# Optimization experiments

Measured on AMD Instinct MI355X. Metric: run time of the kernel, lower is better.

The kernel has to match this reference:

```python
import jax, jax.numpy as jnp
import numpy as np

NUM_HEADS = 16


def setup_inputs() -> dict:
    key = jax.random.key(0)
    k1, k2, k3 = jax.random.split(key, 3)
    b, d, s = 2, 1024, 2048
    x = jax.random.normal(k1, (b, d, s), dtype=jnp.float32)
    # torch nn.Linear(d, 3d) without bias == x @ W1 with W1 of shape (d, 3d)
    W1 = jax.random.normal(k2, (d, 3 * d), dtype=jnp.float32) * (d ** -0.5)
    W2 = jax.random.normal(k3, (d, d), dtype=jnp.float32) * (d ** -0.5)
    return {"x": x, "W1": W1, "W2": W2}


def reference(x, W1, W2):
    # x: (b, hidden_dim, s) -> (b, s, hidden_dim)
    b, d, s = x.shape
    h = NUM_HEADS
    hd = d // h
    xt = jnp.swapaxes(x, 1, 2)                       # (b, s, d)
    qkv = xt @ W1                                    # (b, s, 3d)
    qkv = qkv.reshape(b, s, 3, h, hd)
    qkv = jnp.transpose(qkv, (2, 0, 3, 1, 4))        # (3, b, h, s, hd)
    q, k, v = qkv[0], qkv[1], qkv[2]
    scale = hd ** -0.5
    scores = jnp.einsum("bhqd,bhkd->bhqk", q, k) * scale  # (b, h, s, s)
    # causal mask: same as torch code (adds float32 min where not lower-tri)
    neg = jnp.finfo(jnp.float32).min
    causal = jnp.tril(jnp.ones((s, s), dtype=bool))
    scores = jnp.where(causal[None, None, :, :], scores, scores + neg)
    attn = jax.nn.softmax(scores, axis=-1)           # dropout = identity (eval)
    out = jnp.einsum("bhqk,bhkd->bhqd", attn, v)     # (b, h, s, hd)
    out = jnp.transpose(out, (0, 2, 1, 3)).reshape(b, s, d)
    out = out @ W2                                   # (b, s, d)
    return jnp.swapaxes(out, 1, 2)                   # (b, d, s)
```

## Files before the change

kernel.cpp:

```cpp
#include <hip/hip_runtime.h>
#include <math.h>

#define B_  2
#define D_  1024
#define S_  2048
#define H_  16
#define HD_ 64
#define D3_ 3072
#define M_  4096

typedef __attribute__((ext_vector_type(8))) short short8;
typedef __attribute__((ext_vector_type(4))) float float4v;

__device__ __forceinline__ short f2bf(float f) {
    unsigned u = __builtin_bit_cast(unsigned, f);
    unsigned r = (u + 0x7FFFu + ((u >> 16) & 1u)) >> 16;
    return (short)r;
}

__device__ __forceinline__ unsigned cvt_pk_bf16(float lo, float hi) {
    unsigned r;
    asm("v_cvt_pk_bf16_f32 %0, %1, %2" : "=v"(r) : "v"(lo), "v"(hi));
    return r;
}

__device__ __forceinline__ float fast_exp2(float x) {
    float r;
    asm("v_exp_f32 %0, %1" : "=v"(r) : "v"(x));
    return r;
}

#define GLD16(gsrc, ldst)                                                      \
    __builtin_amdgcn_global_load_lds(                                          \
        (const __attribute__((address_space(1))) void*)(gsrc),                 \
        (__attribute__((address_space(3))) void*)(ldst), 16, 0, 0)

__global__ __launch_bounds__(256) void transpose_cvt(const float* __restrict__ in,
                                                     short* __restrict__ out,
                                                     int R, int C) {
    __shared__ float t[32][33];
    const int c0 = blockIdx.x * 32, r0 = blockIdx.y * 32;
    const float* inb = in + (size_t)blockIdx.z * R * C;
    short* outb = out + (size_t)blockIdx.z * R * C;
    const int tx = threadIdx.x, ty = threadIdx.y;
    #pragma unroll
    for (int i = ty; i < 32; i += 8)
        t[i][tx] = inb[(size_t)(r0 + i) * C + c0 + tx];
    __syncthreads();
    #pragma unroll
    for (int i = ty; i < 32; i += 8)
        outb[(size_t)(c0 + i) * R + r0 + tx] = f2bf(t[tx][i]);
}

__device__ __forceinline__ void gemm_core(const short* __restrict__ A,
                                          const short* __restrict__ Bt,
                                          int m0, int n0,
                                          short* As, short* Bs,
                                          float4v acc[4][4]) {
    const int tid = threadIdx.x;
    const int lane = tid & 63, w = tid >> 6;
    const int wr = (w >> 1) * 64, wc = (w & 1) * 64;
    const int srow = lane >> 2;
    const int scol = (lane & 3) * 8;
    for (int k0 = 0; k0 < 1024; k0 += 32) {
        #pragma unroll
        for (int j = 0; j < 2; ++j) {
            const int ch = 2 * w + j;
            GLD16(A  + (size_t)(m0 + ch * 16 + srow) * 1024 + k0 + scol,
                  As + ch * 512 + lane * 8);
            GLD16(Bt + (size_t)(n0 + ch * 16 + srow) * 1024 + k0 + scol,
                  Bs + ch * 512 + lane * 8);
        }
        __syncthreads();
        short8 a[4], b[4];
        #pragma unroll
        for (int m = 0; m < 4; ++m)
            a[m] = *(const short8*)&As[(wr + m * 16 + (lane & 15)) * 32 + (lane >> 4) * 8];
        #pragma unroll
        for (int n = 0; n < 4; ++n)
            b[n] = *(const short8*)&Bs[(wc + n * 16 + (lane & 15)) * 32 + (lane >> 4) * 8];
        #pragma unroll
        for (int m = 0; m < 4; ++m)
            #pragma unroll
            for (int n = 0; n < 4; ++n)
                acc[m][n] = __builtin_amdgcn_mfma_f32_16x16x32_bf16(a[m], b[n], acc[m][n], 0, 0, 0);
        __syncthreads();
    }
}

__global__ __launch_bounds__(256) void gemm_qkv_mfma(const short* __restrict__ xt,
                                                     const short* __restrict__ W1t,
                                                     short* __restrict__ q,
                                                     short* __restrict__ kk,
                                                     short* __restrict__ vt) {
    __shared__ short As[128 * 32], Bs[128 * 32];
    float4v acc[4][4];
    #pragma unroll
    for (int m = 0; m < 4; ++m)
        #pragma unroll
        for (int n = 0; n < 4; ++n) acc[m][n] = (float4v){0.f, 0.f, 0.f, 0.f};
    const int m0 = blockIdx.y * 128, n0 = blockIdx.x * 128;
    gemm_core(xt, W1t, m0, n0, As, Bs, acc);
    const int lane = threadIdx.x & 63, w = threadIdx.x >> 6;
    const int wr = (w >> 1) * 64, wc = (w & 1) * 64;
    const float qscale = 0.125f * 1.44269504f;
    #pragma unroll
    for (int n = 0; n < 4; ++n) {
        const int gcol = n0 + wc + n * 16 + (lane & 15);
        const int which = gcol >> 10, hh = (gcol >> 6) & 15, hd = gcol & 63;
        #pragma unroll
        for (int m = 0; m < 4; ++m) {
            #pragma unroll
            for (int ri = 0; ri < 4; ++ri) {
                const int grow = m0 + wr + m * 16 + (lane >> 4) * 4 + ri;
                const int bb = grow >> 11, ss = grow & (S_ - 1);
                float av = acc[m][n][ri];
                if (which == 0) av *= qscale;
                const short v = f2bf(av);
                if (which == 0)      q [((size_t)(bb * H_ + hh) * S_ + ss) * HD_ + hd] = v;
                else if (which == 1) kk[((size_t)(bb * H_ + hh) * S_ + ss) * HD_ + hd] = v;
                else                 vt[((size_t)(bb * H_ + hh) * HD_ + hd) * S_ + ss] = v;
            }
        }
    }
}

__global__ __launch_bounds__(256) void attn_mfma(const short* __restrict__ q,
                                                 const short* __restrict__ k,
                                                 const short* __restrict__ vt,
                                                 short* __restrict__ ao) {
    __shared__ short Ks[2][64 * 64];
    __shared__ short Vts[2][64 * 64];
    __shared__ short Ps[64 * 64];
    __shared__ float sums[64];
    const int tid = threadIdx.x;
    const int lane = tid & 63, w = tid >> 6;
    const int bh = blockIdx.y;
    const size_t base = (size_t)bh * S_ * HD_;
    const short* qp = q + base;
    const short* kp = k + base;
    const short* vp = vt + base;
    const int bb = bh >> 4, hh = bh & 15;
    const int wrow = w * 16;

    for (int half = 0; half < 2; ++half) {
        const int qt = (half == 0) ? (int)blockIdx.x : 31 - (int)blockIdx.x;
        const int q0 = qt * 64;
        short8 qf[2];
        #pragma unroll
        for (int ks = 0; ks < 2; ++ks)
            qf[ks] = *(const short8*)&qp[(size_t)(q0 + wrow + (lane & 15)) * HD_
                                         + ks * 32 + (lane >> 4) * 8];
        float4v accO[4];
        float lsum = 0.f;
        #pragma unroll
        for (int n = 0; n < 4; ++n) accO[n] = (float4v){0.f, 0.f, 0.f, 0.f};

        const int nkb = qt + 1;
        __syncthreads();
        #pragma unroll
        for (int j = 0; j < 2; ++j) {
            const int g = (w * 2 + j) * 64 + lane;
            const int r = g >> 3, cs = g & 7;
            const int co = (cs ^ (r & 7)) << 3;
            GLD16(kp + (size_t)r * HD_ + co, &Ks[0][g * 8]);
            GLD16(vp + (size_t)r * S_ + co,  &Vts[0][g * 8]);
        }
        int cur = 0;
        for (int kb = 0; kb < nkb; ++kb) {
            const int kv0 = kb * 64;
            __syncthreads();
            if (kb + 1 < nkb) {
                const int kv1 = kv0 + 64;
                #pragma unroll
                for (int j = 0; j < 2; ++j) {
                    const int g = (w * 2 + j) * 64 + lane;
                    const int r = g >> 3, cs = g & 7;
                    const int co = (cs ^ (r & 7)) << 3;
                    GLD16(kp + (size_t)(kv1 + r) * HD_ + co, &Ks[cur ^ 1][g * 8]);
                    GLD16(vp + (size_t)r * S_ + kv1 + co,    &Vts[cur ^ 1][g * 8]);
                }
            }
            float4v accS[4];
            #pragma unroll
            for (int n = 0; n < 4; ++n) accS[n] = (float4v){0.f, 0.f, 0.f, 0.f};
            #pragma unroll
            for (int ks = 0; ks < 2; ++ks) {
                #pragma unroll
                for (int n = 0; n < 4; ++n) {
                    const int rowk = n * 16 + (lane & 15);
                    const int ch = ks * 4 + (lane >> 4);
                    const short8 kf = *(const short8*)&Ks[cur][rowk * 64 + ((ch ^ (rowk & 7)) << 3)];
                    accS[n] = __builtin_amdgcn_mfma_f32_16x16x32_bf16(kf, qf[ks], accS[n], 0, 0, 0);
                }
            }
            const bool diag = (kb == qt);
            const int qg = q0 + wrow + (lane & 15);
            const int prow = wrow + (lane & 15);
            #pragma unroll
            for (int n = 0; n < 4; ++n) {
                const int kvb = kv0 + n * 16 + ((lane >> 4) << 2);
                float p[4];
                if (diag) {
                    const int dlim = qg - kvb;
                    #pragma unroll
                    for (int ri = 0; ri < 4; ++ri)
                        p[ri] = (ri <= dlim) ? fast_exp2(accS[n][ri]) : 0.f;
                } else {
                    #pragma unroll
                    for (int ri = 0; ri < 4; ++ri)
                        p[ri] = fast_exp2(accS[n][ri]);
                }
                lsum += (p[0] + p[1]) + (p[2] + p[3]);
                const unsigned lo = cvt_pk_bf16(p[0], p[1]);
                const unsigned hi = cvt_pk_bf16(p[2], p[3]);
                const int col = n * 16 + ((lane >> 4) << 2);
                const int ch = col >> 3;
                const int addr = prow * 64 + ((ch ^ (prow & 7)) << 3) + (col & 7);
                *(uint2*)&Ps[addr] = (uint2){lo, hi};
            }
            #pragma unroll
            for (int ks = 0; ks < 2; ++ks) {
                const int prow2 = wrow + (lane & 15);
                const int chp = ks * 4 + (lane >> 4);
                const short8 pf = *(const short8*)&Ps[prow2 * 64 + ((chp ^ (prow2 & 7)) << 3)];
                #pragma unroll
                for (int n = 0; n < 4; ++n) {
                    const int vrow = n * 16 + (lane & 15);
                    const int ch = ks * 4 + (lane >> 4);
                    const short8 vf = *(const short8*)&Vts[cur][vrow * 64 + ((ch ^ (vrow & 7)) << 3)];
                    accO[n] = __builtin_amdgcn_mfma_f32_16x16x32_bf16(pf, vf, accO[n], 0, 0, 0);
                }
            }
            cur ^= 1;
        }
        {
            float t = lsum;
            t += __shfl_xor(t, 16);
            t += __shfl_xor(t, 32);
            if (lane < 16) sums[wrow + lane] = t;
        }
        #pragma unroll
        for (int ri = 0; ri < 4; ++ri) {
            const int lrow = wrow + ((lane >> 4) << 2) + ri;
            const float inv = 1.f / sums[lrow];
            const int grow = q0 + lrow;
            #pragma unroll
            for (int n = 0; n < 4; ++n) {
                const int col = hh * 64 + n * 16 + (lane & 15);
                ao[((size_t)(bb * S_ + grow)) * D_ + col] = f2bf(accO[n][ri] * inv);
            }
        }
    }
}

__global__ __launch_bounds__(256) void gemm_out_mfma(const short* __restrict__ W2t,
                                                     const short* __restrict__ ao,
                                                     float* __restrict__ out) {
    __shared__ short As[128 * 32], Bs[128 * 32];
    float4v acc[4][4];
    #pragma unroll
    for (int m = 0; m < 4; ++m)
        #pragma unroll
        for (int n = 0; n < 4; ++n) acc[m][n] = (float4v){0.f, 0.f, 0.f, 0.f};
    const int m0 = blockIdx.y * 128, n0 = blockIdx.x * 128;
    gemm_core(W2t, ao, m0, n0, As, Bs, acc);
    const int lane = threadIdx.x & 63, w = threadIdx.x >> 6;
    const int wr = (w >> 1) * 64, wc = (w & 1) * 64;
    #pragma unroll
    for (int m = 0; m < 4; ++m) {
        #pragma unroll
        for (int ri = 0; ri < 4; ++ri) {
            const int grow = m0 + wr + m * 16 + (lane >> 4) * 4 + ri;
            #pragma unroll
            for (int n = 0; n < 4; ++n) {
                const int gcol = n0 + wc + n * 16 + (lane & 15);
                const int bb = gcol >> 11, ss = gcol & (S_ - 1);
                out[(size_t)bb * D_ * S_ + (size_t)grow * S_ + ss] = acc[m][n][ri];
            }
        }
    }
}

extern "C" void kernel_launch(void* const* d_in, const int* in_sizes, int n_in,
                              void* d_out, int out_size, void* d_ws, size_t ws_size,
                              hipStream_t stream) {
    const float* x  = (const float*)d_in[0];
    const float* W1 = (const float*)d_in[1];
    const float* W2 = (const float*)d_in[2];
    float* out = (float*)d_out;

    short* xt  = (short*)d_ws;
    short* W1t = xt  + (size_t)M_ * D_;
    short* W2t = W1t + (size_t)D3_ * D_;
    short* q   = W2t + (size_t)D_ * D_;
    short* kk  = q   + (size_t)B_ * H_ * S_ * HD_;
    short* vt  = kk  + (size_t)B_ * H_ * S_ * HD_;
    short* ao  = vt  + (size_t)B_ * H_ * S_ * HD_;

    transpose_cvt<<<dim3(S_ / 32, D_ / 32, B_), dim3(32, 8), 0, stream>>>(x, xt, D_, S_);
    transpose_cvt<<<dim3(D3_ / 32, D_ / 32, 1), dim3(32, 8), 0, stream>>>(W1, W1t, D_, D3_);
    transpose_cvt<<<dim3(D_ / 32, D_ / 32, 1), dim3(32, 8), 0, stream>>>(W2, W2t, D_, D_);
    gemm_qkv_mfma<<<dim3(D3_ / 128, M_ / 128), 256, 0, stream>>>(xt, W1t, q, kk, vt);
    attn_mfma<<<dim3(16, B_ * H_), 256, 0, stream>>>(q, kk, vt, ao);
    gemm_out_mfma<<<dim3(M_ / 128, D_ / 128), 256, 0, stream>>>(W2t, ao, out);
}
```

Measured before the change: 129.6 us.

## Double-buffer GEMM LDS tiles and add XCD-aware block swizzle

```diff
diff --git a/kernel.cpp b/kernel.cpp
--- a/kernel.cpp
+++ b/kernel.cpp
@@ -62,30 +62,47 @@
     const int wr = (w >> 1) * 64, wc = (w & 1) * 64;
     const int srow = lane >> 2;
     const int scol = (lane & 3) * 8;
-    for (int k0 = 0; k0 < 1024; k0 += 32) {
-        #pragma unroll
-        for (int j = 0; j < 2; ++j) {
-            const int ch = 2 * w + j;
-            GLD16(A  + (size_t)(m0 + ch * 16 + srow) * 1024 + k0 + scol,
-                  As + ch * 512 + lane * 8);
-            GLD16(Bt + (size_t)(n0 + ch * 16 + srow) * 1024 + k0 + scol,
-                  Bs + ch * 512 + lane * 8);
-        }
+    #pragma unroll
+    for (int j = 0; j < 2; ++j) {
+        const int ch = 2 * w + j;
+        GLD16(A  + (size_t)(m0 + ch * 16 + srow) * 1024 + scol, As + ch * 512 + lane * 8);
+        GLD16(Bt + (size_t)(n0 + ch * 16 + srow) * 1024 + scol, Bs + ch * 512 + lane * 8);
+    }
+    int cur = 0;
+    for (int t = 0; t < 32; ++t) {
         __syncthreads();
+        if (t + 1 < 32) {
+            const int k1 = (t + 1) * 32;
+            short* Asn = As + (cur ^ 1) * 4096;
+            short* Bsn = Bs + (cur ^ 1) * 4096;
+            #pragma unroll
+            for (int j = 0; j < 2; ++j) {
+                const int ch = 2 * w + j;
+                GLD16(A  + (size_t)(m0 + ch * 16 + srow) * 1024 + k1 + scol, Asn + ch * 512 + lane * 8);
+                GLD16(Bt + (size_t)(n0 + ch * 16 + srow) * 1024 + k1 + scol, Bsn + ch * 512 + lane * 8);
+            }
+        }
+        const short* Asc = As + cur * 4096;
+        const short* Bsc = Bs + cur * 4096;
         short8 a[4], b[4];
         #pragma unroll
         for (int m = 0; m < 4; ++m)
-            a[m] = *(const short8*)&As[(wr + m * 16 + (lane & 15)) * 32 + (lane >> 4) * 8];
+            a[m] = *(const short8*)&Asc[(wr + m * 16 + (lane & 15)) * 32 + (lane >> 4) * 8];
         #pragma unroll
         for (int n = 0; n < 4; ++n)
-            b[n] = *(const short8*)&Bs[(wc + n * 16 + (lane & 15)) * 32 + (lane >> 4) * 8];
+            b[n] = *(const short8*)&Bsc[(wc + n * 16 + (lane & 15)) * 32 + (lane >> 4) * 8];
         #pragma unroll
         for (int m = 0; m < 4; ++m)
             #pragma unroll
             for (int n = 0; n < 4; ++n)
                 acc[m][n] = __builtin_amdgcn_mfma_f32_16x16x32_bf16(a[m], b[n], acc[m][n], 0, 0, 0);
-        __syncthreads();
-    }
+        cur ^= 1;
+    }
+}
+
+__device__ __forceinline__ int xcd_swizzle(int bid, int nwg) {
+    const int cpx = nwg >> 3;
+    return (bid & 7) * cpx + (bid >> 3);
 }
 
 __global__ __launch_bounds__(256) void gemm_qkv_mfma(const short* __restrict__ xt,
@@ -93,14 +110,15 @@
                                                      short* __restrict__ q,
                                                      short* __restrict__ kk,
                                                      short* __restrict__ vt) {
-    __shared__ short As[128 * 32], Bs[128 * 32];
+    __shared__ short As[2][128 * 32], Bs[2][128 * 32];
     float4v acc[4][4];
     #pragma unroll
     for (int m = 0; m < 4; ++m)
         #pragma unroll
         for (int n = 0; n < 4; ++n) acc[m][n] = (float4v){0.f, 0.f, 0.f, 0.f};
-    const int m0 = blockIdx.y * 128, n0 = blockIdx.x * 128;
-    gemm_core(xt, W1t, m0, n0, As, Bs, acc);
+    const int bid = xcd_swizzle((int)blockIdx.x, 24 * 32);
+    const int m0 = (bid / 24) * 128, n0 = (bid % 24) * 128;
+    gemm_core(xt, W1t, m0, n0, &As[0][0], &Bs[0][0], acc);
     const int lane = threadIdx.x & 63, w = threadIdx.x >> 6;
     const int wr = (w >> 1) * 64, wc = (w & 1) * 64;
     const float qscale = 0.125f * 1.44269504f;
@@ -257,14 +275,15 @@
 __global__ __launch_bounds__(256) void gemm_out_mfma(const short* __restrict__ W2t,
                                                      const short* __restrict__ ao,
                                                      float* __restrict__ out) {
-    __shared__ short As[128 * 32], Bs[128 * 32];
+    __shared__ short As[2][128 * 32], Bs[2][128 * 32];
     float4v acc[4][4];
     #pragma unroll
     for (int m = 0; m < 4; ++m)
         #pragma unroll
         for (int n = 0; n < 4; ++n) acc[m][n] = (float4v){0.f, 0.f, 0.f, 0.f};
-    const int m0 = blockIdx.y * 128, n0 = blockIdx.x * 128;
-    gemm_core(W2t, ao, m0, n0, As, Bs, acc);
+    const int bid = xcd_swizzle((int)blockIdx.x, 8 * 32);
+    const int m0 = (bid / 32) * 128, n0 = (bid % 32) * 128;
+    gemm_core(W2t, ao, m0, n0, &As[0][0], &Bs[0][0], acc);
     const int lane = threadIdx.x & 63, w = threadIdx.x >> 6;
     const int wr = (w >> 1) * 64, wc = (w & 1) * 64;
     #pragma unroll
@@ -301,7 +320,7 @@
     transpose_cvt<<<dim3(S_ / 32, D_ / 32, B_), dim3(32, 8), 0, stream>>>(x, xt, D_, S_);
     transpose_cvt<<<dim3(D3_ / 32, D_ / 32, 1), dim3(32, 8), 0, stream>>>(W1, W1t, D_, D3_);
     transpose_cvt<<<dim3(D_ / 32, D_ / 32, 1), dim3(32, 8), 0, stream>>>(W2, W2t, D_, D_);
-    gemm_qkv_mfma<<<dim3(D3_ / 128, M_ / 128), 256, 0, stream>>>(xt, W1t, q, kk, vt);
+    gemm_qkv_mfma<<<dim3(24 * 32), 256, 0, stream>>>(xt, W1t, q, kk, vt);
     attn_mfma<<<dim3(16, B_ * H_), 256, 0, stream>>>(q, kk, vt, ao);
-    gemm_out_mfma<<<dim3(M_ / 128, D_ / 128), 256, 0, stream>>>(W2t, ao, out);
-}
+    gemm_out_mfma<<<dim3(8 * 32), 256, 0, stream>>>(W2t, ao, out);
+}
```

After: 137.2 us. 1.06x slower.

## Double GEMM K-tile to 64 with XOR-swizzled LDS and remap attention blocks per XCD

Applied to the files above, without the earlier changes.

```diff
diff --git a/kernel.cpp b/kernel.cpp
--- a/kernel.cpp
+++ b/kernel.cpp
@@ -60,30 +60,37 @@
     const int tid = threadIdx.x;
     const int lane = tid & 63, w = tid >> 6;
     const int wr = (w >> 1) * 64, wc = (w & 1) * 64;
-    const int srow = lane >> 2;
-    const int scol = (lane & 3) * 8;
-    for (int k0 = 0; k0 < 1024; k0 += 32) {
-        #pragma unroll
-        for (int j = 0; j < 2; ++j) {
-            const int ch = 2 * w + j;
-            GLD16(A  + (size_t)(m0 + ch * 16 + srow) * 1024 + k0 + scol,
-                  As + ch * 512 + lane * 8);
-            GLD16(Bt + (size_t)(n0 + ch * 16 + srow) * 1024 + k0 + scol,
-                  Bs + ch * 512 + lane * 8);
+    for (int k0 = 0; k0 < 1024; k0 += 64) {
+        #pragma unroll
+        for (int j = 0; j < 4; ++j) {
+            const int g = j * 256 + tid;
+            const int r = g >> 3, cs = g & 7;
+            const int co = (cs ^ (r & 7)) << 3;
+            GLD16(A  + (size_t)(m0 + r) * 1024 + k0 + co, As + g * 8);
+            GLD16(Bt + (size_t)(n0 + r) * 1024 + k0 + co, Bs + g * 8);
         }
         __syncthreads();
-        short8 a[4], b[4];
-        #pragma unroll
-        for (int m = 0; m < 4; ++m)
-            a[m] = *(const short8*)&As[(wr + m * 16 + (lane & 15)) * 32 + (lane >> 4) * 8];
-        #pragma unroll
-        for (int n = 0; n < 4; ++n)
-            b[n] = *(const short8*)&Bs[(wc + n * 16 + (lane & 15)) * 32 + (lane >> 4) * 8];
-        #pragma unroll
-        for (int m = 0; m < 4; ++m)
-            #pragma unroll
-            for (int n = 0; n < 4; ++n)
-                acc[m][n] = __builtin_amdgcn_mfma_f32_16x16x32_bf16(a[m], b[n], acc[m][n], 0, 0, 0);
+        #pragma unroll
+        for (int ks = 0; ks < 2; ++ks) {
+            short8 a[4], b[4];
+            #pragma unroll
+            for (int m = 0; m < 4; ++m) {
+                const int row = wr + m * 16 + (lane & 15);
+                const int ch = ks * 4 + (lane >> 4);
+                a[m] = *(const short8*)&As[row * 64 + ((ch ^ (row & 7)) << 3)];
+            }
+            #pragma unroll
+            for (int n = 0; n < 4; ++n) {
+                const int row = wc + n * 16 + (lane & 15);
+                const int ch = ks * 4 + (lane >> 4);
+                b[n] = *(const short8*)&Bs[row * 64 + ((ch ^ (row & 7)) << 3)];
+            }
+            #pragma unroll
+            for (int m = 0; m < 4; ++m)
+                #pragma unroll
+                for (int n = 0; n < 4; ++n)
+                    acc[m][n] = __builtin_amdgcn_mfma_f32_16x16x32_bf16(a[m], b[n], acc[m][n], 0, 0, 0);
+        }
         __syncthreads();
     }
 }
@@ -93,7 +100,7 @@
                                                      short* __restrict__ q,
                                                      short* __restrict__ kk,
                                                      short* __restrict__ vt) {
-    __shared__ short As[128 * 32], Bs[128 * 32];
+    __shared__ short As[128 * 64], Bs[128 * 64];
     float4v acc[4][4];
     #pragma unroll
     for (int m = 0; m < 4; ++m)
@@ -135,7 +142,10 @@
     __shared__ float sums[64];
     const int tid = threadIdx.x;
     const int lane = tid & 63, w = tid >> 6;
-    const int bh = blockIdx.y;
+    const int bid = (int)blockIdx.x;
+    const int xcd = bid & 7, slot = bid >> 3;
+    const int bh = xcd * 4 + (slot & 3);
+    const int qpair = slot >> 2;
     const size_t base = (size_t)bh * S_ * HD_;
     const short* qp = q + base;
     const short* kp = k + base;
@@ -144,7 +154,7 @@
     const int wrow = w * 16;
 
     for (int half = 0; half < 2; ++half) {
-        const int qt = (half == 0) ? (int)blockIdx.x : 31 - (int)blockIdx.x;
+        const int qt = (half == 0) ? qpair : 31 - qpair;
         const int q0 = qt * 64;
         short8 qf[2];
         #pragma unroll
@@ -257,7 +267,7 @@
 __global__ __launch_bounds__(256) void gemm_out_mfma(const short* __restrict__ W2t,
                                                      const short* __restrict__ ao,
                                                      float* __restrict__ out) {
-    __shared__ short As[128 * 32], Bs[128 * 32];
+    __shared__ short As[128 * 64], Bs[128 * 64];
     float4v acc[4][4];
     #pragma unroll
     for (int m = 0; m < 4; ++m)
@@ -302,6 +312,6 @@
     transpose_cvt<<<dim3(D3_ / 32, D_ / 32, 1), dim3(32, 8), 0, stream>>>(W1, W1t, D_, D3_);
     transpose_cvt<<<dim3(D_ / 32, D_ / 32, 1), dim3(32, 8), 0, stream>>>(W2, W2t, D_, D_);
     gemm_qkv_mfma<<<dim3(D3_ / 128, M_ / 128), 256, 0, stream>>>(xt, W1t, q, kk, vt);
-    attn_mfma<<<dim3(16, B_ * H_), 256, 0, stream>>>(q, kk, vt, ao);
+    attn_mfma<<<dim3(512), 256, 0, stream>>>(q, kk, vt, ao);
     gemm_out_mfma<<<dim3(M_ / 128, D_ / 128), 256, 0, stream>>>(W2t, ao, out);
 }
```

Result: slower. 134.0 us (+3.4%).

## Process paired short and long query tiles together to share K/V loads

Applied to the files above, without the earlier changes.

```diff
diff --git a/kernel.cpp b/kernel.cpp
--- a/kernel.cpp
+++ b/kernel.cpp
@@ -131,10 +131,11 @@
                                                  short* __restrict__ ao) {
     __shared__ short Ks[2][64 * 64];
     __shared__ short Vts[2][64 * 64];
-    __shared__ short Ps[64 * 64];
-    __shared__ float sums[64];
+    __shared__ short Ps[128 * 64];
+    __shared__ float sums[128];
     const int tid = threadIdx.x;
     const int lane = tid & 63, w = tid >> 6;
+    const int qpair = blockIdx.x;
     const int bh = blockIdx.y;
     const size_t base = (size_t)bh * S_ * HD_;
     const short* qp = q + base;
@@ -143,60 +144,72 @@
     const int bb = bh >> 4, hh = bh & 15;
     const int wrow = w * 16;
 
-    for (int half = 0; half < 2; ++half) {
-        const int qt = (half == 0) ? (int)blockIdx.x : 31 - (int)blockIdx.x;
-        const int q0 = qt * 64;
-        short8 qf[2];
-        #pragma unroll
-        for (int ks = 0; ks < 2; ++ks)
-            qf[ks] = *(const short8*)&qp[(size_t)(q0 + wrow + (lane & 15)) * HD_
-                                         + ks * 32 + (lane >> 4) * 8];
-        float4v accO[4];
-        float lsum = 0.f;
-        #pragma unroll
-        for (int n = 0; n < 4; ++n) accO[n] = (float4v){0.f, 0.f, 0.f, 0.f};
-
-        const int nkb = qt + 1;
+    const int qtS = qpair, qtL = 31 - qpair;
+    const int q0S = qtS * 64, q0L = qtL * 64;
+    const int nkbL = qtL + 1;
+
+    short8 qfS[2], qfL[2];
+    #pragma unroll
+    for (int ks = 0; ks < 2; ++ks) {
+        qfS[ks] = *(const short8*)&qp[(size_t)(q0S + wrow + (lane & 15)) * HD_
+                                      + ks * 32 + (lane >> 4) * 8];
+        qfL[ks] = *(const short8*)&qp[(size_t)(q0L + wrow + (lane & 15)) * HD_
+                                      + ks * 32 + (lane >> 4) * 8];
+    }
+    float4v accOS[4], accOL[4];
+    float lsumS = 0.f, lsumL = 0.f;
+    #pragma unroll
+    for (int n = 0; n < 4; ++n) {
+        accOS[n] = (float4v){0.f, 0.f, 0.f, 0.f};
+        accOL[n] = (float4v){0.f, 0.f, 0.f, 0.f};
+    }
+
+    #pragma unroll
+    for (int j = 0; j < 2; ++j) {
+        const int g = (w * 2 + j) * 64 + lane;
+        const int r = g >> 3, cs = g & 7;
+        const int co = (cs ^ (r & 7)) << 3;
+        GLD16(kp + (size_t)r * HD_ + co, &Ks[0][g * 8]);
+        GLD16(vp + (size_t)r * S_ + co,  &Vts[0][g * 8]);
+    }
+    int cur = 0;
+    for (int kb = 0; kb < nkbL; ++kb) {
+        const int kv0 = kb * 64;
         __syncthreads();
-        #pragma unroll
-        for (int j = 0; j < 2; ++j) {
-            const int g = (w * 2 + j) * 64 + lane;
-            const int r = g >> 3, cs = g & 7;
-            const int co = (cs ^ (r & 7)) << 3;
-            GLD16(kp + (size_t)r * HD_ + co, &Ks[0][g * 8]);
-            GLD16(vp + (size_t)r * S_ + co,  &Vts[0][g * 8]);
-        }
-        int cur = 0;
-        for (int kb = 0; kb < nkb; ++kb) {
-            const int kv0 = kb * 64;
-            __syncthreads();
-            if (kb + 1 < nkb) {
-                const int kv1 = kv0 + 64;
-                #pragma unroll
-                for (int j = 0; j < 2; ++j) {
-                    const int g = (w * 2 + j) * 64 + lane;
-                    const int r = g >> 3, cs = g & 7;
-                    const int co = (cs ^ (r & 7)) << 3;
-                    GLD16(kp + (size_t)(kv1 + r) * HD_ + co, &Ks[cur ^ 1][g * 8]);
-                    GLD16(vp + (size_t)r * S_ + kv1 + co,    &Vts[cur ^ 1][g * 8]);
-                }
-            }
-            float4v accS[4];
-            #pragma unroll
-            for (int n = 0; n < 4; ++n) accS[n] = (float4v){0.f, 0.f, 0.f, 0.f};
-            #pragma unroll
-            for (int ks = 0; ks < 2; ++ks) {
-                #pragma unroll
-                for (int n = 0; n < 4; ++n) {
-                    const int rowk = n * 16 + (lane & 15);
-                    const int ch = ks * 4 + (lane >> 4);
-                    const short8 kf = *(const short8*)&Ks[cur][rowk * 64 + ((ch ^ (rowk & 7)) << 3)];
-                    accS[n] = __builtin_amdgcn_mfma_f32_16x16x32_bf16(kf, qf[ks], accS[n], 0, 0, 0);
-                }
-            }
-            const bool diag = (kb == qt);
-            const int qg = q0 + wrow + (lane & 15);
-            const int prow = wrow + (lane & 15);
+        if (kb + 1 < nkbL) {
+            const int kv1 = kv0 + 64;
+            #pragma unroll
+            for (int j = 0; j < 2; ++j) {
+                const int g = (w * 2 + j) * 64 + lane;
+                const int r = g >> 3, cs = g & 7;
+                const int co = (cs ^ (r & 7)) << 3;
+                GLD16(kp + (size_t)(kv1 + r) * HD_ + co, &Ks[cur ^ 1][g * 8]);
+                GLD16(vp + (size_t)r * S_ + kv1 + co,    &Vts[cur ^ 1][g * 8]);
+            }
+        }
+        const bool actS = (kb <= qtS);
+        float4v scS[4], scL[4];
+        #pragma unroll
+        for (int n = 0; n < 4; ++n) {
+            scS[n] = (float4v){0.f, 0.f, 0.f, 0.f};
+            scL[n] = (float4v){0.f, 0.f, 0.f, 0.f};
+        }
+        #pragma unroll
+        for (int ks = 0; ks < 2; ++ks) {
+            #pragma unroll
+            for (int n = 0; n < 4; ++n) {
+                const int rowk = n * 16 + (lane & 15);
+                const int ch = ks * 4 + (lane >> 4);
+                const short8 kf = *(const short8*)&Ks[cur][rowk * 64 + ((ch ^ (rowk & 7)) << 3)];
+                scL[n] = __builtin_amdgcn_mfma_f32_16x16x32_bf16(kf, qfL[ks], scL[n], 0, 0, 0);
+                if (actS)
+                    scS[n] = __builtin_amdgcn_mfma_f32_16x16x32_bf16(kf, qfS[ks], scS[n], 0, 0, 0);
+            }
+        }
+        {
+            const bool diag = (kb == qtL);
+            const int qg = q0L + wrow + (lane & 15);
+            const int prow = 64 + wrow + (lane & 15);
             #pragma unroll
             for (int n = 0; n < 4; ++n) {
                 const int kvb = kv0 + n * 16 + ((lane >> 4) << 2);
@@ -205,13 +218,13 @@
                     const int dlim = qg - kvb;
                     #pragma unroll
                     for (int ri = 0; ri < 4; ++ri)
-                        p[ri] = (ri <= dlim) ? fast_exp2(accS[n][ri]) : 0.f;
+                        p[ri] = (ri <= dlim) ? fast_exp2(scL[n][ri]) : 0.f;
                 } else {
                     #pragma unroll
                     for (int ri = 0; ri < 4; ++ri)
-                        p[ri] = fast_exp2(accS[n][ri]);
+                        p[ri] = fast_exp2(scL[n][ri]);
                 }
-                lsum += (p[0] + p[1]) + (p[2] + p[3]);
+                lsumL += (p[0] + p[1]) + (p[2] + p[3]);
                 const unsigned lo = cvt_pk_bf16(p[0], p[1]);
                 const unsigned hi = cvt_pk_bf16(p[2], p[3]);
                 const int col = n * 16 + ((lane >> 4) << 2);
@@ -219,37 +232,80 @@
                 const int addr = prow * 64 + ((ch ^ (prow & 7)) << 3) + (col & 7);
                 *(uint2*)&Ps[addr] = (uint2){lo, hi};
             }
-            #pragma unroll
-            for (int ks = 0; ks < 2; ++ks) {
-                const int prow2 = wrow + (lane & 15);
-                const int chp = ks * 4 + (lane >> 4);
-                const short8 pf = *(const short8*)&Ps[prow2 * 64 + ((chp ^ (prow2 & 7)) << 3)];
-                #pragma unroll
-                for (int n = 0; n < 4; ++n) {
-                    const int vrow = n * 16 + (lane & 15);
-                    const int ch = ks * 4 + (lane >> 4);
-                    const short8 vf = *(const short8*)&Vts[cur][vrow * 64 + ((ch ^ (vrow & 7)) << 3)];
-                    accO[n] = __builtin_amdgcn_mfma_f32_16x16x32_bf16(pf, vf, accO[n], 0, 0, 0);
+        }
+        if (actS) {
+            const bool diag = (kb == qtS);
+            const int qg = q0S + wrow + (lane & 15);
+            const int prow = wrow + (lane & 15);
+            #pragma unroll
+            for (int n = 0; n < 4; ++n) {
+                const int kvb = kv0 + n * 16 + ((lane >> 4) << 2);
+                float p[4];
+                if (diag) {
+                    const int dlim = qg - kvb;
+                    #pragma unroll
+                    for (int ri = 0; ri < 4; ++ri)
+                        p[ri] = (ri <= dlim) ? fast_exp2(scS[n][ri]) : 0.f;
+                } else {
+                    #pragma unroll
+                    for (int ri = 0; ri < 4; ++ri)
+                        p[ri] = fast_exp2(scS[n][ri]);
                 }
-            }
-            cur ^= 1;
-        }
-        {
-            float t = lsum;
-            t += __shfl_xor(t, 16);
-            t += __shfl_xor(t, 32);
-            if (lane < 16) sums[wrow + lane] = t;
-        }
-        #pragma unroll
-        for (int ri = 0; ri < 4; ++ri) {
-            const int lrow = wrow + ((lane >> 4) << 2) + ri;
-            const float inv = 1.f / sums[lrow];
-            const int grow = q0 + lrow;
-            #pragma unroll
-            for (int n = 0; n < 4; ++n) {
-                const int col = hh * 64 + n * 16 + (lane & 15);
-                ao[((size_t)(bb * S_ + grow)) * D_ + col] = f2bf(accO[n][ri] * inv);
-            }
+                lsumS += (p[0] + p[1]) + (p[2] + p[3]);
+                const unsigned lo = cvt_pk_bf16(p[0], p[1]);
+                const unsigned hi = cvt_pk_bf16(p[2], p[3]);
+                const int col = n * 16 + ((lane >> 4) << 2);
+                const int ch = col >> 3;
+                const int addr = prow * 64 + ((ch ^ (prow & 7)) << 3) + (col & 7);
+                *(uint2*)&Ps[addr] = (uint2){lo, hi};
+            }
+        }
+        #pragma unroll
+        for (int ks = 0; ks < 2; ++ks) {
+            const int chp = ks * 4 + (lane >> 4);
+            const int prowL = 64 + wrow + (lane & 15);
+            const short8 pfL = *(const short8*)&Ps[prowL * 64 + ((chp ^ (prowL & 7)) << 3)];
+            short8 pfS;
+            if (actS) {
+                const int prowS = wrow + (lane & 15);
+                pfS = *(const short8*)&Ps[prowS * 64 + ((chp ^ (prowS & 7)) << 3)];
+            }
+            #pragma unroll
+            for (int n = 0; n < 4; ++n) {
+                const int vrow = n * 16 + (lane & 15);
+                const int ch = ks * 4 + (lane >> 4);
+                const short8 vf = *(const short8*)&Vts[cur][vrow * 64 + ((ch ^ (vrow & 7)) << 3)];
+                accOL[n] = __builtin_amdgcn_mfma_f32_16x16x32_bf16(pfL, vf, accOL[n], 0, 0, 0);
+                if (actS)
+                    accOS[n] = __builtin_amdgcn_mfma_f32_16x16x32_bf16(pfS, vf, accOS[n], 0, 0, 0);
+            }
+        }
+        cur ^= 1;
+    }
+    {
+        float t = lsumS;
+        t += __shfl_xor(t, 16);
+        t += __shfl_xor(t, 32);
+        if (lane < 16) sums[wrow + lane] = t;
+    }
+    {
+        float t = lsumL;
+        t += __shfl_xor(t, 16);
+        t += __shfl_xor(t, 32);
+        if (lane < 16) sums[64 + wrow + lane] = t;
+    }
+    #pragma unroll
+    for (int ri = 0; ri < 4; ++ri) {
+        const int lrow = wrow + ((lane >> 4) << 2) + ri;
+        const float invS = 1.f / sums[lrow];
+        const float invL = 1.f / sums[64 + lrow];
+        const int growS = q0S + lrow;
+        const int growL = q0L + lrow;
+        #pragma unroll
+        for (int n = 0; n < 4; ++n) {
+            const int col = hh * 64 + n * 16 + (lane & 15);
+            ao[((size_t)(bb * S_ + growS)) * D_ + col] = f2bf(accOS[n][ri] * invS);
+            ao[((size_t)(bb * S_ + growL)) * D_ + col] = f2bf(accOL[n][ri] * invL);
         }
     }
 }
```

Result: slower. 141.8 us (+9.4%).
